# Optimization experiments

Hardware: AMD Instinct MI355X
Metric: run time of the kernel (lower is better)

## Reference

```python
import jax, jax.numpy as jnp
import numpy as np
import math

HID, HEADS, HD = 1024, 16, 64
DFF = 4 * HID
EPS = 1e-6
RES_SCALE = 0.5

def build_alibi_slopes(n_heads):
    def get_slopes(power):
        start = 2 ** (-2 ** (-(math.log2(power) - 3)))
        return [start * start ** i for i in range(power)]
    if math.log2(n_heads).is_integer():
        slopes = get_slopes(n_heads)
    else:
        closest = 2 ** math.floor(math.log2(n_heads))
        slopes = get_slopes(closest)
        extra = get_slopes(2 * closest)
        slopes = slopes + extra[0::2][: n_heads - closest]
    return jnp.asarray(np.array(slopes, dtype=np.float32))

def rmsnorm(x, w):
    var = jnp.mean(x * x, axis=-1, keepdims=True)
    return x * jax.lax.rsqrt(var + EPS) * w

def setup_inputs() -> dict:
    key = jax.random.key(0)
    ks = jax.random.split(key, 12)
    s = lambda d: 1.0 / math.sqrt(d)
    return {
        "x": jax.random.normal(ks[0], (2, 2048, HID), dtype=jnp.float32),
        "norm1_w": jnp.ones((HID,), jnp.float32),
        "Wq": jax.random.normal(ks[1], (HID, HEADS * HD), jnp.float32) * s(HID),
        "bq": jax.random.normal(ks[2], (HEADS * HD,), jnp.float32) * 0.01,
        "Wk": jax.random.normal(ks[3], (HID, HEADS * HD), jnp.float32) * s(HID),
        "bk": jax.random.normal(ks[4], (HEADS * HD,), jnp.float32) * 0.01,
        "Wv": jax.random.normal(ks[5], (HID, HEADS * HD), jnp.float32) * s(HID),
        "Wo": jax.random.normal(ks[6], (HEADS * HD, HID), jnp.float32) * s(HEADS * HD),
        "norm2_w": jnp.ones((HID,), jnp.float32),
        "W1": jax.random.normal(ks[7], (HID, DFF), jnp.float32) * s(HID),
        "b1": jax.random.normal(ks[8], (DFF,), jnp.float32) * 0.01,
        "W2": jax.random.normal(ks[9], (DFF, HID), jnp.float32) * s(DFF),
        "b2": jax.random.normal(ks[10], (HID,), jnp.float32) * 0.01,
    }

def reference(x, norm1_w, Wq, bq, Wk, bk, Wv, Wo, norm2_w, W1, b1, W2, b2):
    b, s, _ = x.shape
    scale = HD ** -0.5
    xn = rmsnorm(x, norm1_w)
    q = (xn @ Wq + bq).reshape(b, s, HEADS, HD).transpose(0, 2, 1, 3)
    k = (xn @ Wk + bk).reshape(b, s, HEADS, HD).transpose(0, 2, 1, 3)
    v = (xn @ Wv).reshape(b, s, HEADS, HD).transpose(0, 2, 1, 3)
    scores = jnp.einsum('bhqd,bhkd->bhqk', q, k) * scale
    pos = jnp.arange(s)
    dist = jnp.abs(pos[None, :] - pos[:, None]).astype(scores.dtype)  # [s,s]
    slopes = build_alibi_slopes(HEADS)
    bias = -slopes[:, None, None] * dist[None, :, :]  # [h,s,s]
    scores = scores + bias[None]
    weights = jax.nn.softmax(scores, axis=-1)
    attn = jnp.einsum('bhqk,bhkd->bhqd', weights, v)
    attn = attn.transpose(0, 2, 1, 3).reshape(b, s, HEADS * HD)
    x = x + attn @ Wo
    xn2 = rmsnorm(x, norm2_w)
    h = jax.nn.gelu(xn2 @ W1 + b1, approximate=False)
    x = x + RES_SCALE * (h @ W2 + b2)
    return x
```

## Files before the change

### kernel.cpp

```cpp
#include <hip/hip_runtime.h>
#include <hip/hip_bf16.h>
#include <math.h>

#define S_LEN   2048
#define HIDN    1024
#define NHEADS  16
#define HDIM    64
#define NTOK    4096
#define DFFN    4096

#define LOG2E 1.44269504088896f

typedef __attribute__((ext_vector_type(8))) __bf16 bf16x8;
typedef __attribute__((ext_vector_type(4))) float  f32x4;

static __device__ __forceinline__ ushort f2bf(float f) {
  union { float f; unsigned u; } v; v.f = f;
  unsigned u = v.u;
  unsigned r = (u + 0x7fffu + ((u >> 16) & 1u)) >> 16;
  return (ushort)r;
}
static __device__ __forceinline__ ushort f2bf_fast(float f) {
  union { float f; unsigned u; } v; v.f = f;
  return (ushort)((v.u + 0x8000u) >> 16);
}

#define GLOAD16(gp, lp)                                                              \
  __builtin_amdgcn_global_load_lds((const __attribute__((address_space(1))) void*)(gp), \
                                   (__attribute__((address_space(3))) void*)(lp), 16, 0, 0)

__global__ __launch_bounds__(256) void convert_wT(const float* __restrict__ W,
                                                  ushort* __restrict__ WT,
                                                  int K, int N) {
  __shared__ float tile[32][33];
  int n0 = blockIdx.x * 32, k0 = blockIdx.y * 32;
  int tx = threadIdx.x & 31, ty = threadIdx.x >> 5;
#pragma unroll
  for (int i = 0; i < 4; i++)
    tile[ty + i * 8][tx] = W[(size_t)(k0 + ty + i * 8) * N + n0 + tx];
  __syncthreads();
#pragma unroll
  for (int i = 0; i < 4; i++)
    WT[(size_t)(n0 + ty + i * 8) * K + k0 + tx] = f2bf(tile[tx][ty + i * 8]);
}

__global__ void build_bias(const float* __restrict__ bq, const float* __restrict__ bk,
                           float* __restrict__ biasqkv) {
  int i = blockIdx.x * 256 + threadIdx.x;
  if (i < 3 * HIDN) {
    float v = (i < HIDN) ? bq[i] : (i < 2 * HIDN ? bk[i - HIDN] : 0.0f);
    biasqkv[i] = v;
  }
}

__global__ __launch_bounds__(256) void rmsnorm_kernel(const float* __restrict__ x,
                                                      const float* __restrict__ w,
                                                      ushort* __restrict__ out) {
  int row = blockIdx.x, t = threadIdx.x;
  const float4* x4 = (const float4*)(x + (size_t)row * HIDN);
  float4 v = x4[t];
  float ss = v.x * v.x + v.y * v.y + v.z * v.z + v.w * v.w;
#pragma unroll
  for (int m = 32; m; m >>= 1) ss += __shfl_xor(ss, m, 64);
  __shared__ float wsum[4];
  if ((t & 63) == 0) wsum[t >> 6] = ss;
  __syncthreads();
  float tot = wsum[0] + wsum[1] + wsum[2] + wsum[3];
  float rs = rsqrtf(tot * (1.0f / HIDN) + 1e-6f);
  const float4* w4 = (const float4*)w;
  float4 wv = w4[t];
  ushort4 o;
  o.x = f2bf(v.x * rs * wv.x);
  o.y = f2bf(v.y * rs * wv.y);
  o.z = f2bf(v.z * rs * wv.z);
  o.w = f2bf(v.w * rs * wv.w);
  *(ushort4*)(out + (size_t)row * HIDN + t * 4) = o;
}

template <int EPI, int TM>
__global__ __launch_bounds__(256, 3) void gemm_bt(const ushort* __restrict__ A,
                                                  const ushort* __restrict__ B,
                                                  int M, int N, int K,
                                                  const float* __restrict__ bias,
                                                  const float* __restrict__ resid,
                                                  float* __restrict__ outf,
                                                  ushort* __restrict__ outb,
                                                  ushort* __restrict__ qb,
                                                  ushort* __restrict__ kb,
                                                  ushort* __restrict__ vb) {
  constexpr int NF = (TM == 128) ? 4 : 2;
  __shared__ __align__(16) ushort As[TM * 64];
  __shared__ __align__(16) ushort Bs[128 * 64];
  int t = threadIdx.x;
  int w = t >> 6, l = t & 63;
  int wmr = (TM == 128) ? (w >> 1) * 64 : 0;
  int wnc = (TM == 128) ? (w & 1) * 64 : w * 32;
  int lr = l & 15, lg = l >> 4;
  int m0 = blockIdx.x * TM, n0 = blockIdx.y * 128;

  int srl = l >> 3;
  int sg  = ((l & 7) ^ srl) * 8;
  const ushort* Ag = A + (size_t)(m0 + w * (TM / 4) + srl) * K + sg;
  const ushort* Bg = B + (size_t)(n0 + w * 32 + srl) * K + sg;
  ushort* Asw = &As[(w * (TM / 4)) * 64];
  ushort* Bsw = &Bs[(w * 32) * 64];

  f32x4 acc[4][NF] = {};

  for (int k0 = 0; k0 < K; k0 += 64) {
#pragma unroll
    for (int c = 0; c < TM / 32; c++)
      GLOAD16(Ag + (size_t)(8 * c) * K + k0, Asw + (8 * c) * 64);
#pragma unroll
    for (int c = 0; c < 4; c++)
      GLOAD16(Bg + (size_t)(8 * c) * K + k0, Bsw + (8 * c) * 64);
    __syncthreads();

    bf16x8 af[4][2], bfr[NF][2];
#pragma unroll
    for (int mf = 0; mf < 4; mf++)
#pragma unroll
      for (int ks = 0; ks < 2; ks++)
        af[mf][ks] = *(const bf16x8*)(&As[(wmr + mf * 16 + lr) * 64 +
                                          (((ks * 4 + lg) ^ (lr & 7)) << 3)]);
#pragma unroll
    for (int nf = 0; nf < NF; nf++)
#pragma unroll
      for (int ks = 0; ks < 2; ks++)
        bfr[nf][ks] = *(const bf16x8*)(&Bs[(wnc + nf * 16 + lr) * 64 +
                                           (((ks * 4 + lg) ^ (lr & 7)) << 3)]);
#pragma unroll
    for (int mf = 0; mf < 4; mf++)
#pragma unroll
      for (int nf = 0; nf < NF; nf++) {
        acc[mf][nf] = __builtin_amdgcn_mfma_f32_16x16x32_bf16(af[mf][0], bfr[nf][0], acc[mf][nf], 0, 0, 0);
        acc[mf][nf] = __builtin_amdgcn_mfma_f32_16x16x32_bf16(af[mf][1], bfr[nf][1], acc[mf][nf], 0, 0, 0);
      }
    __syncthreads();
  }

  int lg4 = lg * 4;
  if constexpr (EPI == 0) {
#pragma unroll
    for (int mf = 0; mf < 4; mf++) {
      int row0 = m0 + wmr + mf * 16 + lg4;
      int bb = row0 >> 11, ss0 = row0 & 2047;
#pragma unroll
      for (int nf = 0; nf < NF; nf++) {
        int col = n0 + wnc + nf * 16 + lr;
        float bcol = bias[col];
        int which = col >> 10, nn = col & 1023;
        int hh = nn >> 6, dd = nn & 63;
        if (which == 2) {
          ushort4 o;
          o.x = f2bf(acc[mf][nf][0] + bcol);
          o.y = f2bf(acc[mf][nf][1] + bcol);
          o.z = f2bf(acc[mf][nf][2] + bcol);
          o.w = f2bf(acc[mf][nf][3] + bcol);
          *(ushort4*)(vb + ((size_t)(bb * NHEADS + hh) * HDIM + dd) * S_LEN + ss0) = o;
        } else {
#pragma unroll
          for (int r = 0; r < 4; r++) {
            float v = acc[mf][nf][r] + bcol;
            size_t idx = ((size_t)(bb * NHEADS + hh) * S_LEN + ss0 + r) * HDIM + dd;
            if (which == 0) qb[idx] = f2bf(v * (0.125f * LOG2E));
            else kb[idx] = f2bf(v);
          }
        }
      }
    }
  } else {
#pragma unroll
    for (int mf = 0; mf < 4; mf++) {
#pragma unroll
      for (int nf = 0; nf < NF; nf++) {
#pragma unroll
        for (int r = 0; r < 4; r++) {
          int row = m0 + wmr + mf * 16 + lg4 + r;
          int col = n0 + wnc + nf * 16 + lr;
          float v = acc[mf][nf][r];
          if constexpr (EPI == 1) {
            outf[(size_t)row * HIDN + col] = resid[(size_t)row * HIDN + col] + v;
          } else if constexpr (EPI == 2) {
            float tv = v + bias[col];
            float gl = 0.5f * tv * (1.0f + erff(tv * 0.70710678118f));
            outb[(size_t)row * DFFN + col] = f2bf(gl);
          } else {
            outf[(size_t)row * HIDN + col] =
                resid[(size_t)row * HIDN + col] + 0.5f * (v + bias[col]);
          }
        }
      }
    }
  }
}

__global__ __launch_bounds__(256, 3) void attn_kernel(const ushort* __restrict__ qb,
                                                      const ushort* __restrict__ kb,
                                                      const ushort* __restrict__ vt,
                                                      ushort* __restrict__ attn_out) {
  __shared__ __align__(16) ushort Ks[2][64 * 64];
  __shared__ __align__(16) ushort VTs[2][64 * 64];
  __shared__ __align__(16) ushort Ps[4][16 * 72];
  int t = threadIdx.x;
  int w = t >> 6, l = t & 63;
  int lr = l & 15, lg = l >> 4, g8 = lg * 8;
  int blk = blockIdx.x;
  int qt = blk & 31;
  int bh = blk >> 5;
  int h = bh & 15;
  float slope2 = exp2f(-0.5f * (float)(h + 1)) * LOG2E;
  float s64 = slope2 * 64.0f;
  int q0 = qt * 64;
  const ushort* qp = qb + (size_t)bh * S_LEN * HDIM;

  int srow = w * 16 + (l >> 3);
  int sgr  = ((l & 7) ^ (l >> 3)) * 8;
  const ushort* kbase = kb + (size_t)bh * S_LEN * HDIM + (size_t)srow * HDIM + sgr;
  const ushort* vbase = vt + (size_t)bh * HDIM * S_LEN + (size_t)srow * S_LEN + sgr;

  auto stage = [&](int tile, int b) {
    const ushort* ksrc = kbase + (size_t)tile * 64 * HDIM;
    const ushort* vsrc = vbase + tile * 64;
    GLOAD16(ksrc,                       &Ks[b][(w * 16) * 64]);
    GLOAD16(ksrc + 8 * HDIM,            &Ks[b][(w * 16 + 8) * 64]);
    GLOAD16(vsrc,                       &VTs[b][(w * 16) * 64]);
    GLOAD16(vsrc + (size_t)8 * S_LEN,   &VTs[b][(w * 16 + 8) * 64]);
  };

  bf16x8 qf[2];
#pragma unroll
  for (int ks = 0; ks < 2; ks++)
    qf[ks] = *(const bf16x8*)(qp + (size_t)(q0 + w * 16 + lr) * HDIM + ks * 32 + g8);

  f32x4 ao[4] = {};
  float mrow[4] = {-INFINITY, -INFINITY, -INFINITY, -INFINITY};
  float lden[4] = {0.f, 0.f, 0.f, 0.f};

  f32x4 biasv[4];
  if (qt > 0) {
#pragma unroll
    for (int nf = 0; nf < 4; nf++)
#pragma unroll
      for (int r = 0; r < 4; r++)
        biasv[nf][r] = -slope2 * (float)(q0 + w * 16 + lg * 4 + r - nf * 16 - lr);
  }

  stage(0, 0);
  __syncthreads();

  for (int tt = 0; tt < S_LEN / 64; tt++) {
    int cur = tt & 1;
    if (tt + 1 < S_LEN / 64) stage(tt + 1, cur ^ 1);

    bool diag = (tt == qt);

    f32x4 sc[4];
#pragma unroll
    for (int nf = 0; nf < 4; nf++) {
      f32x4 a = diag ? f32x4{0.f, 0.f, 0.f, 0.f} : biasv[nf];
#pragma unroll
      for (int ks = 0; ks < 2; ks++) {
        bf16x8 kf = *(const bf16x8*)(&Ks[cur][(nf * 16 + lr) * 64 +
                                             (((ks * 4 + lg) ^ (lr & 7)) << 3)]);
        a = __builtin_amdgcn_mfma_f32_16x16x32_bf16(qf[ks], kf, a, 0, 0, 0);
      }
      sc[nf] = a;
    }

    if (diag) {
#pragma unroll
      for (int nf = 0; nf < 4; nf++) {
        float kk = (float)(nf * 16 + lr);
#pragma unroll
        for (int r = 0; r < 4; r++) {
          float qq = (float)(w * 16 + lg * 4 + r);
          sc[nf][r] -= slope2 * fabsf(qq - kk);
        }
      }
#pragma unroll
      for (int nf = 0; nf < 4; nf++)
#pragma unroll
        for (int r = 0; r < 4; r++)
          biasv[nf][r] = -slope2 * (float)(64 + nf * 16 + lr - w * 16 - lg * 4 - r);
    }

    float pmax[4];
#pragma unroll
    for (int r = 0; r < 4; r++) {
      float mx = fmaxf(fmaxf(sc[0][r], sc[1][r]), fmaxf(sc[2][r], sc[3][r]));
#pragma unroll
      for (int m = 1; m < 16; m <<= 1) mx = fmaxf(mx, __shfl_xor(mx, m, 64));
      pmax[r] = mx;
    }

    int need = 0;
#pragma unroll
    for (int r = 0; r < 4; r++) need |= (pmax[r] > mrow[r]);
    if (__any(need)) {
#pragma unroll
      for (int r = 0; r < 4; r++) {
        float mn = fmaxf(mrow[r], pmax[r]);
        float scl = exp2f(mrow[r] - mn);
        mrow[r] = mn;
        lden[r] *= scl;
#pragma unroll
        for (int nf = 0; nf < 4; nf++) ao[nf][r] *= scl;
      }
    }

#pragma unroll
    for (int r = 0; r < 4; r++) {
      float su = 0.f;
#pragma unroll
      for (int nf = 0; nf < 4; nf++) {
        float p = exp2f(sc[nf][r] - mrow[r]);
        sc[nf][r] = p;
        su += p;
      }
#pragma unroll
      for (int m = 1; m < 16; m <<= 1) su += __shfl_xor(su, m, 64);
      lden[r] += su;
    }
#pragma unroll
    for (int nf = 0; nf < 4; nf++)
#pragma unroll
      for (int r = 0; r < 4; r++)
        Ps[w][(lg * 4 + r) * 72 + nf * 16 + lr] = f2bf_fast(sc[nf][r]);
    asm volatile("s_waitcnt lgkmcnt(0)" ::: "memory");
    __builtin_amdgcn_sched_barrier(0);

    bf16x8 pf[2];
#pragma unroll
    for (int ks = 0; ks < 2; ks++)
      pf[ks] = *(const bf16x8*)(&Ps[w][lr * 72 + ks * 32 + g8]);
#pragma unroll
    for (int nf = 0; nf < 4; nf++) {
#pragma unroll
      for (int ks = 0; ks < 2; ks++) {
        bf16x8 vf = *(const bf16x8*)(&VTs[cur][(nf * 16 + lr) * 64 +
                                              (((ks * 4 + lg) ^ (lr & 7)) << 3)]);
        ao[nf] = __builtin_amdgcn_mfma_f32_16x16x32_bf16(pf[ks], vf, ao[nf], 0, 0, 0);
      }
    }

    int next = tt + 1;
    if (!diag && next != qt) {
      float d = (next < qt) ? s64 : -s64;
#pragma unroll
      for (int nf = 0; nf < 4; nf++)
#pragma unroll
        for (int r = 0; r < 4; r++) biasv[nf][r] += d;
    }
    __syncthreads();
  }

  int token_base = (bh >> 4) * S_LEN + q0 + w * 16;
#pragma unroll
  for (int nf = 0; nf < 4; nf++) {
#pragma unroll
    for (int r = 0; r < 4; r++) {
      int token = token_base + lg * 4 + r;
      int d = nf * 16 + lr;
      attn_out[(size_t)token * HIDN + h * HDIM + d] = f2bf(ao[nf][r] / lden[r]);
    }
  }
}

extern "C" void kernel_launch(void* const* d_in, const int* in_sizes, int n_in,
                              void* d_out, int out_size, void* d_ws, size_t ws_size,
                              hipStream_t stream) {
  const float* x   = (const float*)d_in[0];
  const float* n1w = (const float*)d_in[1];
  const float* Wq  = (const float*)d_in[2];
  const float* bq  = (const float*)d_in[3];
  const float* Wk  = (const float*)d_in[4];
  const float* bk  = (const float*)d_in[5];
  const float* Wv  = (const float*)d_in[6];
  const float* Wo  = (const float*)d_in[7];
  const float* n2w = (const float*)d_in[8];
  const float* W1  = (const float*)d_in[9];
  const float* b1  = (const float*)d_in[10];
  const float* W2  = (const float*)d_in[11];
  const float* b2  = (const float*)d_in[12];
  float* out = (float*)d_out;

  char* ws = (char*)d_ws;
  ushort* xn     = (ushort*)(ws + 0);
  ushort* wqkvT  = (ushort*)(ws + 8388608);
  ushort* woT    = (ushort*)(ws + 14680064);
  ushort* w1T    = (ushort*)(ws + 16777216);
  ushort* w2T    = (ushort*)(ws + 25165824);
  float*  biasq  = (float*)(ws + 33554432);
  ushort* qbuf   = (ushort*)(ws + 33566720);
  ushort* kbuf   = (ushort*)(ws + 41955328);
  ushort* vtbuf  = (ushort*)(ws + 50343936);
  ushort* attnb  = (ushort*)(ws + 58732544);
  float*  x2     = (float*)(ws + 67121152);
  ushort* xn2    = (ushort*)(ws + 83898368);
  ushort* hbuf   = qbuf;

  dim3 blk(256);

  convert_wT<<<dim3(32, 32), blk, 0, stream>>>(Wq, wqkvT, HIDN, HIDN);
  convert_wT<<<dim3(32, 32), blk, 0, stream>>>(Wk, wqkvT + 1024 * 1024, HIDN, HIDN);
  convert_wT<<<dim3(32, 32), blk, 0, stream>>>(Wv, wqkvT + 2 * 1024 * 1024, HIDN, HIDN);
  convert_wT<<<dim3(32, 32), blk, 0, stream>>>(Wo, woT, HIDN, HIDN);
  convert_wT<<<dim3(128, 32), blk, 0, stream>>>(W1, w1T, HIDN, DFFN);
  convert_wT<<<dim3(32, 128), blk, 0, stream>>>(W2, w2T, DFFN, HIDN);
  build_bias<<<12, blk, 0, stream>>>(bq, bk, biasq);

  rmsnorm_kernel<<<NTOK, blk, 0, stream>>>(x, n1w, xn);
  gemm_bt<0, 128><<<dim3(32, 24), blk, 0, stream>>>(xn, wqkvT, NTOK, 3 * HIDN, HIDN,
                                                    biasq, nullptr, nullptr, nullptr,
                                                    qbuf, kbuf, vtbuf);
  attn_kernel<<<dim3(32 * 32), blk, 0, stream>>>(qbuf, kbuf, vtbuf, attnb);
  gemm_bt<1, 64><<<dim3(64, 8), blk, 0, stream>>>(attnb, woT, NTOK, HIDN, HIDN,
                                                  nullptr, x, x2, nullptr,
                                                  nullptr, nullptr, nullptr);
  rmsnorm_kernel<<<NTOK, blk, 0, stream>>>(x2, n2w, xn2);
  gemm_bt<2, 128><<<dim3(32, 32), blk, 0, stream>>>(xn2, w1T, NTOK, DFFN, HIDN,
                                                    b1, nullptr, nullptr, hbuf,
                                                    nullptr, nullptr, nullptr);
  gemm_bt<3, 64><<<dim3(64, 8), blk, 0, stream>>>(hbuf, w2T, NTOK, HIDN, DFFN,
                                                  b2, x2, out, nullptr,
                                                  nullptr, nullptr, nullptr);
}
```

Measured before the change: 453.2 us.

## Fuse weight conversions, swizzle workgroups, keep attention P in registers

Merges the six weight-transpose launches and the bias-build kernel into one launch, and passes bq/bk straight to the QKV GEMM epilogue. Adds XCD-aware block-index swizzling to the GEMMs and attention. Attention now computes S transposed (K as the A operand) so each lane holds per-query-column values. Softmax then needs only two shuffles per reduction, and P is converted to bf16 operands in registers instead of going through shared memory. It also sets s_setprio around the MFMA blocks and raises the occupancy hint, which adds register pressure and depends on correct fragment-layout remapping.

```diff
diff --git a/kernel.cpp b/kernel.cpp
--- a/kernel.cpp
+++ b/kernel.cpp
@@ -20,20 +20,33 @@
   unsigned r = (u + 0x7fffu + ((u >> 16) & 1u)) >> 16;
   return (ushort)r;
 }
-static __device__ __forceinline__ ushort f2bf_fast(float f) {
-  union { float f; unsigned u; } v; v.f = f;
-  return (ushort)((v.u + 0x8000u) >> 16);
-}
 
 #define GLOAD16(gp, lp)                                                              \
   __builtin_amdgcn_global_load_lds((const __attribute__((address_space(1))) void*)(gp), \
                                    (__attribute__((address_space(3))) void*)(lp), 16, 0, 0)
 
-__global__ __launch_bounds__(256) void convert_wT(const float* __restrict__ W,
-                                                  ushort* __restrict__ WT,
-                                                  int K, int N) {
+__global__ __launch_bounds__(256) void convert_all(const float* __restrict__ Wq,
+                                                   const float* __restrict__ Wk,
+                                                   const float* __restrict__ Wv,
+                                                   const float* __restrict__ Wo,
+                                                   const float* __restrict__ W1,
+                                                   const float* __restrict__ W2,
+                                                   ushort* __restrict__ wqkvT,
+                                                   ushort* __restrict__ woT,
+                                                   ushort* __restrict__ w1T,
+                                                   ushort* __restrict__ w2T) {
   __shared__ float tile[32][33];
-  int n0 = blockIdx.x * 32, k0 = blockIdx.y * 32;
+  int id = blockIdx.x;
+  const float* W; ushort* WT; int K, N, tl;
+  if (id < 3072) {
+    int i = id >> 10; tl = id & 1023;
+    W = (i == 0) ? Wq : (i == 1) ? Wk : Wv;
+    WT = wqkvT + i * 1024 * 1024; K = 1024; N = 1024;
+  } else if (id < 4096) { tl = id - 3072; W = Wo; WT = woT; K = 1024; N = 1024; }
+  else if (id < 8192)   { tl = id - 4096; W = W1; WT = w1T; K = 1024; N = 4096; }
+  else                  { tl = id - 8192; W = W2; WT = w2T; K = 4096; N = 1024; }
+  int ntn = N >> 5;
+  int n0 = (tl % ntn) * 32, k0 = (tl / ntn) * 32;
   int tx = threadIdx.x & 31, ty = threadIdx.x >> 5;
 #pragma unroll
   for (int i = 0; i < 4; i++)
@@ -42,15 +55,6 @@
 #pragma unroll
   for (int i = 0; i < 4; i++)
     WT[(size_t)(n0 + ty + i * 8) * K + k0 + tx] = f2bf(tile[tx][ty + i * 8]);
-}
-
-__global__ void build_bias(const float* __restrict__ bq, const float* __restrict__ bk,
-                           float* __restrict__ biasqkv) {
-  int i = blockIdx.x * 256 + threadIdx.x;
-  if (i < 3 * HIDN) {
-    float v = (i < HIDN) ? bq[i] : (i < 2 * HIDN ? bk[i - HIDN] : 0.0f);
-    biasqkv[i] = v;
-  }
 }
 
 __global__ __launch_bounds__(256) void rmsnorm_kernel(const float* __restrict__ x,
@@ -96,7 +100,12 @@
   int wmr = (TM == 128) ? (w >> 1) * 64 : 0;
   int wnc = (TM == 128) ? (w & 1) * 64 : w * 32;
   int lr = l & 15, lg = l >> 4;
-  int m0 = blockIdx.x * TM, n0 = blockIdx.y * 128;
+
+  int nwg = gridDim.x * gridDim.y;
+  int bid = blockIdx.y * gridDim.x + blockIdx.x;
+  int swz = (bid & 7) * (nwg >> 3) + (bid >> 3);
+  int bx = swz % gridDim.x, by = swz / gridDim.x;
+  int m0 = bx * TM, n0 = by * 128;
 
   int srl = l >> 3;
   int sg  = ((l & 7) ^ srl) * 8;
@@ -148,15 +157,15 @@
 #pragma unroll
       for (int nf = 0; nf < NF; nf++) {
         int col = n0 + wnc + nf * 16 + lr;
-        float bcol = bias[col];
         int which = col >> 10, nn = col & 1023;
         int hh = nn >> 6, dd = nn & 63;
+        float bcol = (which == 0) ? bias[nn] : (which == 1) ? resid[nn] : 0.0f;
         if (which == 2) {
           ushort4 o;
-          o.x = f2bf(acc[mf][nf][0] + bcol);
-          o.y = f2bf(acc[mf][nf][1] + bcol);
-          o.z = f2bf(acc[mf][nf][2] + bcol);
-          o.w = f2bf(acc[mf][nf][3] + bcol);
+          o.x = f2bf(acc[mf][nf][0]);
+          o.y = f2bf(acc[mf][nf][1]);
+          o.z = f2bf(acc[mf][nf][2]);
+          o.w = f2bf(acc[mf][nf][3]);
           *(ushort4*)(vb + ((size_t)(bb * NHEADS + hh) * HDIM + dd) * S_LEN + ss0) = o;
         } else {
 #pragma unroll
@@ -195,37 +204,42 @@
   }
 }
 
-__global__ __launch_bounds__(256, 3) void attn_kernel(const ushort* __restrict__ qb,
+__global__ __launch_bounds__(256, 4) void attn_kernel(const ushort* __restrict__ qb,
                                                       const ushort* __restrict__ kb,
                                                       const ushort* __restrict__ vt,
                                                       ushort* __restrict__ attn_out) {
   __shared__ __align__(16) ushort Ks[2][64 * 64];
   __shared__ __align__(16) ushort VTs[2][64 * 64];
-  __shared__ __align__(16) ushort Ps[4][16 * 72];
   int t = threadIdx.x;
   int w = t >> 6, l = t & 63;
   int lr = l & 15, lg = l >> 4, g8 = lg * 8;
-  int blk = blockIdx.x;
+
+  int nwg = gridDim.x;
+  int bid = blockIdx.x;
+  int blk = (bid & 7) * (nwg >> 3) + (bid >> 3);
   int qt = blk & 31;
   int bh = blk >> 5;
   int h = bh & 15;
   float slope2 = exp2f(-0.5f * (float)(h + 1)) * LOG2E;
-  float s64 = slope2 * 64.0f;
+  float s64v = slope2 * 64.0f;
   int q0 = qt * 64;
   const ushort* qp = qb + (size_t)bh * S_LEN * HDIM;
-
-  int srow = w * 16 + (l >> 3);
-  int sgr  = ((l & 7) ^ (l >> 3)) * 8;
-  const ushort* kbase = kb + (size_t)bh * S_LEN * HDIM + (size_t)srow * HDIM + sgr;
-  const ushort* vbase = vt + (size_t)bh * HDIM * S_LEN + (size_t)srow * S_LEN + sgr;
+  const ushort* kp = kb + (size_t)bh * S_LEN * HDIM;
+  const ushort* vp = vt + (size_t)bh * HDIM * S_LEN;
+
+  int S0 = (l >> 3) & 3;
+  size_t kof0 = (size_t)(w * 16 + (l >> 3)) * HDIM + (size_t)(((l & 7) ^ S0) * 8);
+  size_t kof1 = (size_t)(w * 16 + 8 + (l >> 3)) * HDIM + (size_t)(((l & 7) ^ S0 ^ 4) * 8);
+  size_t vof0 = (size_t)(w * 16 + (l >> 3)) * S_LEN + (size_t)(((l & 7) ^ S0) * 8);
+  size_t vof1 = (size_t)(w * 16 + 8 + (l >> 3)) * S_LEN + (size_t)(((l & 7) ^ S0 ^ 4) * 8);
 
   auto stage = [&](int tile, int b) {
-    const ushort* ksrc = kbase + (size_t)tile * 64 * HDIM;
-    const ushort* vsrc = vbase + tile * 64;
-    GLOAD16(ksrc,                       &Ks[b][(w * 16) * 64]);
-    GLOAD16(ksrc + 8 * HDIM,            &Ks[b][(w * 16 + 8) * 64]);
-    GLOAD16(vsrc,                       &VTs[b][(w * 16) * 64]);
-    GLOAD16(vsrc + (size_t)8 * S_LEN,   &VTs[b][(w * 16 + 8) * 64]);
+    const ushort* ks_ = kp + (size_t)tile * 64 * HDIM;
+    const ushort* vs_ = vp + tile * 64;
+    GLOAD16(ks_ + kof0, &Ks[b][(w * 16) * 64]);
+    GLOAD16(ks_ + kof1, &Ks[b][(w * 16 + 8) * 64]);
+    GLOAD16(vs_ + vof0, &VTs[b][(w * 16) * 64]);
+    GLOAD16(vs_ + vof1, &VTs[b][(w * 16 + 8) * 64]);
   };
 
   bf16x8 qf[2];
@@ -234,17 +248,21 @@
     qf[ks] = *(const bf16x8*)(qp + (size_t)(q0 + w * 16 + lr) * HDIM + ks * 32 + g8);
 
   f32x4 ao[4] = {};
-  float mrow[4] = {-INFINITY, -INFINITY, -INFINITY, -INFINITY};
-  float lden[4] = {0.f, 0.f, 0.f, 0.f};
-
+  float mrow = -INFINITY, lden = 0.f;
+
+  int qabs = q0 + w * 16 + lr;
   f32x4 biasv[4];
   if (qt > 0) {
 #pragma unroll
     for (int nf = 0; nf < 4; nf++)
 #pragma unroll
       for (int r = 0; r < 4; r++)
-        biasv[nf][r] = -slope2 * (float)(q0 + w * 16 + lg * 4 + r - nf * 16 - lr);
+        biasv[nf][r] = -slope2 * (float)(qabs - (32 * (nf >> 1) + 8 * lg + 4 * (nf & 1) + r));
   }
+
+  int kbase_row = ((lr >> 2) << 3) + (lr & 3);
+  int SK = (lr & 3) | (((lr >> 2) & 1) << 2);
+  int SV = (lr & 3) | (((lr >> 3) & 1) << 2);
 
   stage(0, 0);
   __syncthreads();
@@ -252,109 +270,103 @@
   for (int tt = 0; tt < S_LEN / 64; tt++) {
     int cur = tt & 1;
     if (tt + 1 < S_LEN / 64) stage(tt + 1, cur ^ 1);
-
     bool diag = (tt == qt);
 
     f32x4 sc[4];
+    __builtin_amdgcn_s_setprio(1);
 #pragma unroll
     for (int nf = 0; nf < 4; nf++) {
+      int kvr = kbase_row + ((nf & 1) << 2) + ((nf >> 1) << 5);
       f32x4 a = diag ? f32x4{0.f, 0.f, 0.f, 0.f} : biasv[nf];
 #pragma unroll
       for (int ks = 0; ks < 2; ks++) {
-        bf16x8 kf = *(const bf16x8*)(&Ks[cur][(nf * 16 + lr) * 64 +
-                                             (((ks * 4 + lg) ^ (lr & 7)) << 3)]);
-        a = __builtin_amdgcn_mfma_f32_16x16x32_bf16(qf[ks], kf, a, 0, 0, 0);
+        bf16x8 kf = *(const bf16x8*)(&Ks[cur][kvr * 64 + (((ks * 4 + lg) ^ SK) << 3)]);
+        a = __builtin_amdgcn_mfma_f32_16x16x32_bf16(kf, qf[ks], a, 0, 0, 0);
       }
       sc[nf] = a;
     }
+    __builtin_amdgcn_s_setprio(0);
 
     if (diag) {
-#pragma unroll
-      for (int nf = 0; nf < 4; nf++) {
-        float kk = (float)(nf * 16 + lr);
+      int qq = w * 16 + lr;
+#pragma unroll
+      for (int nf = 0; nf < 4; nf++)
 #pragma unroll
         for (int r = 0; r < 4; r++) {
-          float qq = (float)(w * 16 + lg * 4 + r);
-          sc[nf][r] -= slope2 * fabsf(qq - kk);
+          int kvloc = 32 * (nf >> 1) + 8 * lg + 4 * (nf & 1) + r;
+          sc[nf][r] -= slope2 * fabsf((float)(qq - kvloc));
+          biasv[nf][r] = -slope2 * (float)(64 + kvloc - qq);
         }
-      }
+    }
+
+    float mx = -INFINITY;
+#pragma unroll
+    for (int nf = 0; nf < 4; nf++)
+#pragma unroll
+      for (int r = 0; r < 4; r++) mx = fmaxf(mx, sc[nf][r]);
+    mx = fmaxf(mx, __shfl_xor(mx, 16, 64));
+    mx = fmaxf(mx, __shfl_xor(mx, 32, 64));
+
+    if (__any(mx > mrow)) {
+      float mn = fmaxf(mrow, mx);
+      float scl = exp2f(mrow - mn);
+      mrow = mn;
+      lden *= scl;
+      float so[4];
+#pragma unroll
+      for (int r = 0; r < 4; r++) so[r] = __shfl(scl, lg * 4 + r, 64);
 #pragma unroll
       for (int nf = 0; nf < 4; nf++)
 #pragma unroll
-        for (int r = 0; r < 4; r++)
-          biasv[nf][r] = -slope2 * (float)(64 + nf * 16 + lr - w * 16 - lg * 4 - r);
-    }
-
-    float pmax[4];
-#pragma unroll
-    for (int r = 0; r < 4; r++) {
-      float mx = fmaxf(fmaxf(sc[0][r], sc[1][r]), fmaxf(sc[2][r], sc[3][r]));
-#pragma unroll
-      for (int m = 1; m < 16; m <<= 1) mx = fmaxf(mx, __shfl_xor(mx, m, 64));
-      pmax[r] = mx;
-    }
-
-    int need = 0;
-#pragma unroll
-    for (int r = 0; r < 4; r++) need |= (pmax[r] > mrow[r]);
-    if (__any(need)) {
+        for (int r = 0; r < 4; r++) ao[nf][r] *= so[r];
+    }
+
+    float su = 0.f;
+#pragma unroll
+    for (int nf = 0; nf < 4; nf++)
 #pragma unroll
       for (int r = 0; r < 4; r++) {
-        float mn = fmaxf(mrow[r], pmax[r]);
-        float scl = exp2f(mrow[r] - mn);
-        mrow[r] = mn;
-        lden[r] *= scl;
-#pragma unroll
-        for (int nf = 0; nf < 4; nf++) ao[nf][r] *= scl;
-      }
-    }
-
-#pragma unroll
-    for (int r = 0; r < 4; r++) {
-      float su = 0.f;
-#pragma unroll
-      for (int nf = 0; nf < 4; nf++) {
-        float p = exp2f(sc[nf][r] - mrow[r]);
+        float p = exp2f(sc[nf][r] - mrow);
         sc[nf][r] = p;
         su += p;
       }
-#pragma unroll
-      for (int m = 1; m < 16; m <<= 1) su += __shfl_xor(su, m, 64);
-      lden[r] += su;
-    }
-#pragma unroll
-    for (int nf = 0; nf < 4; nf++)
-#pragma unroll
-      for (int r = 0; r < 4; r++)
-        Ps[w][(lg * 4 + r) * 72 + nf * 16 + lr] = f2bf_fast(sc[nf][r]);
-    asm volatile("s_waitcnt lgkmcnt(0)" ::: "memory");
-    __builtin_amdgcn_sched_barrier(0);
+    su += __shfl_xor(su, 16, 64);
+    su += __shfl_xor(su, 32, 64);
+    lden += su;
 
     bf16x8 pf[2];
 #pragma unroll
     for (int ks = 0; ks < 2; ks++)
-      pf[ks] = *(const bf16x8*)(&Ps[w][lr * 72 + ks * 32 + g8]);
+#pragma unroll
+      for (int j = 0; j < 8; j++)
+        pf[ks][j] = (__bf16)sc[2 * ks + (j >> 2)][j & 3];
+
+    __builtin_amdgcn_s_setprio(1);
 #pragma unroll
     for (int nf = 0; nf < 4; nf++) {
+      int d = nf * 16 + lr;
 #pragma unroll
       for (int ks = 0; ks < 2; ks++) {
-        bf16x8 vf = *(const bf16x8*)(&VTs[cur][(nf * 16 + lr) * 64 +
-                                              (((ks * 4 + lg) ^ (lr & 7)) << 3)]);
+        bf16x8 vf = *(const bf16x8*)(&VTs[cur][d * 64 + (((ks * 4 + lg) ^ SV) << 3)]);
         ao[nf] = __builtin_amdgcn_mfma_f32_16x16x32_bf16(pf[ks], vf, ao[nf], 0, 0, 0);
       }
     }
+    __builtin_amdgcn_s_setprio(0);
 
     int next = tt + 1;
     if (!diag && next != qt) {
-      float d = (next < qt) ? s64 : -s64;
+      float dd = (next < qt) ? s64v : -s64v;
 #pragma unroll
       for (int nf = 0; nf < 4; nf++)
 #pragma unroll
-        for (int r = 0; r < 4; r++) biasv[nf][r] += d;
+        for (int r = 0; r < 4; r++) biasv[nf][r] += dd;
     }
     __syncthreads();
   }
 
+  float inv[4];
+#pragma unroll
+  for (int r = 0; r < 4; r++) inv[r] = 1.0f / __shfl(lden, lg * 4 + r, 64);
   int token_base = (bh >> 4) * S_LEN + q0 + w * 16;
 #pragma unroll
   for (int nf = 0; nf < 4; nf++) {
@@ -362,7 +374,7 @@
     for (int r = 0; r < 4; r++) {
       int token = token_base + lg * 4 + r;
       int d = nf * 16 + lr;
-      attn_out[(size_t)token * HIDN + h * HDIM + d] = f2bf(ao[nf][r] / lden[r]);
+      attn_out[(size_t)token * HIDN + h * HDIM + d] = f2bf(ao[nf][r] * inv[r]);
     }
   }
 }
@@ -391,7 +403,6 @@
   ushort* woT    = (ushort*)(ws + 14680064);
   ushort* w1T    = (ushort*)(ws + 16777216);
   ushort* w2T    = (ushort*)(ws + 25165824);
-  float*  biasq  = (float*)(ws + 33554432);
   ushort* qbuf   = (ushort*)(ws + 33566720);
   ushort* kbuf   = (ushort*)(ws + 41955328);
   ushort* vtbuf  = (ushort*)(ws + 50343936);
@@ -402,17 +413,11 @@
 
   dim3 blk(256);
 
-  convert_wT<<<dim3(32, 32), blk, 0, stream>>>(Wq, wqkvT, HIDN, HIDN);
-  convert_wT<<<dim3(32, 32), blk, 0, stream>>>(Wk, wqkvT + 1024 * 1024, HIDN, HIDN);
-  convert_wT<<<dim3(32, 32), blk, 0, stream>>>(Wv, wqkvT + 2 * 1024 * 1024, HIDN, HIDN);
-  convert_wT<<<dim3(32, 32), blk, 0, stream>>>(Wo, woT, HIDN, HIDN);
-  convert_wT<<<dim3(128, 32), blk, 0, stream>>>(W1, w1T, HIDN, DFFN);
-  convert_wT<<<dim3(32, 128), blk, 0, stream>>>(W2, w2T, DFFN, HIDN);
-  build_bias<<<12, blk, 0, stream>>>(bq, bk, biasq);
-
+  convert_all<<<dim3(12288), blk, 0, stream>>>(Wq, Wk, Wv, Wo, W1, W2,
+                                               wqkvT, woT, w1T, w2T);
   rmsnorm_kernel<<<NTOK, blk, 0, stream>>>(x, n1w, xn);
   gemm_bt<0, 128><<<dim3(32, 24), blk, 0, stream>>>(xn, wqkvT, NTOK, 3 * HIDN, HIDN,
-                                                    biasq, nullptr, nullptr, nullptr,
+                                                    bq, bk, nullptr, nullptr,
                                                     qbuf, kbuf, vtbuf);
   attn_kernel<<<dim3(32 * 32), blk, 0, stream>>>(qbuf, kbuf, vtbuf, attnb);
   gemm_bt<1, 64><<<dim3(64, 8), blk, 0, stream>>>(attnb, woT, NTOK, HIDN, HIDN,
```

Result: faster. 382.0 us (-15.7%).
